# Optimization experiments

Hardware: AMD Instinct MI355X
Metric: run time of the kernel (lower is better)

The kernel has to match this reference:

```python
import jax, jax.numpy as jnp
import numpy as np

N_USERS = 100000
N_ITEMS = 200000
N_NODES = N_USERS + N_ITEMS
LATENT_DIM = 64
N_LAYERS = 3
NNZ = 6400000


def setup_inputs() -> dict:
    key = jax.random.key(0)
    k1, k2, k3, k4, k5 = jax.random.split(key, 5)
    user_emb = 0.1 * jax.random.normal(k1, (N_USERS, LATENT_DIM), dtype=jnp.float32)
    item_emb = 0.1 * jax.random.normal(k2, (N_ITEMS, LATENT_DIM), dtype=jnp.float32)
    rows = jax.random.randint(k3, (NNZ,), 0, N_NODES, dtype=jnp.int32)
    cols = jax.random.randint(k4, (NNZ,), 0, N_NODES, dtype=jnp.int32)
    # normalized-adjacency-like positive values
    vals = jax.random.uniform(k5, (NNZ,), dtype=jnp.float32) * 0.05
    return {"user_emb": user_emb, "item_emb": item_emb,
            "rows": rows, "cols": cols, "vals": vals}


def _spmm(rows, cols, vals, x):
    # y[r] += vals[e] * x[cols[e]]  for each edge e with rows[e]==r
    gathered = vals[:, None] * x[cols]          # [nnz, D]
    return jax.ops.segment_sum(gathered, rows, num_segments=N_NODES)


def reference(user_emb, item_emb, rows, cols, vals):
    # LightGCN.computer(): multi-hop propagation + layer mean pooling
    all_emb = jnp.concatenate([user_emb, item_emb], axis=0)   # [N, D]
    acc = all_emb
    for _ in range(N_LAYERS):
        all_emb = _spmm(rows, cols, vals, all_emb)
        acc = acc + all_emb
    light_out = acc / (N_LAYERS + 1)
    users = light_out[:N_USERS]
    items = light_out[N_USERS:]
    return users, items
```

## Files before the change

### kernel.cpp

```cpp
#include <hip/hip_runtime.h>
#include <hip/hip_bf16.h>

#define N_USERS 100000
#define N_ITEMS 200000
#define N_NODES 300000
#define DIM 64

#define TOT_ELEMS ((size_t)N_NODES * DIM)
#define TOT_F4    (TOT_ELEMS / 4)
#define USER_F4   (((size_t)N_USERS * DIM) / 4)

#define BROWS 512
#define NBUCKET ((N_NODES + BROWS - 1) / BROWS)
#define EPT 32
#define EDGES_PER_BLOCK (EPT * 256)

typedef float f4_native __attribute__((ext_vector_type(4)));

__device__ __forceinline__ float bf2f(unsigned short u) {
    return __uint_as_float((unsigned int)u << 16);
}
__device__ __forceinline__ unsigned short f2bf(float f) {
    __hip_bfloat16 h = __float2bfloat16(f);
    return *reinterpret_cast<unsigned short*>(&h);
}
__device__ __forceinline__ float lo_bf(unsigned int u) {
    return __uint_as_float(u << 16);
}
__device__ __forceinline__ float hi_bf(unsigned int u) {
    return __uint_as_float(u & 0xFFFF0000u);
}

__global__ void init_kernel(const float* __restrict__ user,
                            const float* __restrict__ item,
                            ushort4* __restrict__ xh) {
    size_t i = (size_t)blockIdx.x * blockDim.x + threadIdx.x;
    if (i >= TOT_F4) return;
    f4_native v = (i < USER_F4)
        ? __builtin_nontemporal_load((const f4_native*)user + i)
        : __builtin_nontemporal_load((const f4_native*)item + (i - USER_F4));
    ushort4 h;
    h.x = f2bf(v.x); h.y = f2bf(v.y); h.z = f2bf(v.z); h.w = f2bf(v.w);
    xh[i] = h;
}

__global__ void zero_buckets_kernel(int* __restrict__ bucket_count) {
    int i = blockIdx.x * blockDim.x + threadIdx.x;
    if (i < NBUCKET) bucket_count[i] = 0;
}

__global__ void bucket_hist_kernel(const int* __restrict__ rows,
                                   int* __restrict__ bucket_count, int nnz) {
    __shared__ int h[NBUCKET];
    int t = threadIdx.x;
    size_t base = (size_t)blockIdx.x * EDGES_PER_BLOCK;
    for (int i = t; i < NBUCKET; i += 256) h[i] = 0;
    __syncthreads();
    #pragma unroll 4
    for (int k = 0; k < EPT; ++k) {
        size_t e = base + (size_t)k * 256 + t;
        if (e < (size_t)nnz) atomicAdd(&h[rows[e] >> 9], 1);
    }
    __syncthreads();
    for (int i = t; i < NBUCKET; i += 256) {
        int c = h[i];
        if (c) atomicAdd(&bucket_count[i], c);
    }
}

__global__ void bucket_scan_kernel(const int* __restrict__ bucket_count,
                                   int* __restrict__ bucket_base,
                                   int* __restrict__ bucket_cursor, int nnz) {
    __shared__ int s[1024];
    int t = threadIdx.x;
    int orig = (t < NBUCKET) ? bucket_count[t] : 0;
    s[t] = orig;
    __syncthreads();
    for (int off = 1; off < 1024; off <<= 1) {
        int v = (t >= off) ? s[t - off] : 0;
        __syncthreads();
        s[t] += v;
        __syncthreads();
    }
    if (t < NBUCKET) {
        int excl = s[t] - orig;
        bucket_base[t]   = excl;
        bucket_cursor[t] = excl;
    }
    if (t == 0) bucket_base[NBUCKET] = nnz;
}

__global__ void binA_kernel(const int* __restrict__ rows,
                            const int* __restrict__ cols,
                            const float* __restrict__ vals,
                            int* __restrict__ bucket_cursor,
                            int2* __restrict__ binned,
                            int nnz) {
    __shared__ int  h[NBUCKET];
    __shared__ int  lstart[NBUCKET];
    __shared__ int  lcur[NBUCKET];
    __shared__ int  gbase[NBUCKET];
    __shared__ int  s[256];
    __shared__ int2 ledge[EDGES_PER_BLOCK];

    int t = threadIdx.x;
    size_t base = (size_t)blockIdx.x * EDGES_PER_BLOCK;
    int nvalid = (int)(((size_t)nnz - base < (size_t)EDGES_PER_BLOCK)
                       ? ((size_t)nnz - base) : (size_t)EDGES_PER_BLOCK);

    for (int i = t; i < NBUCKET; i += 256) h[i] = 0;
    __syncthreads();

    #pragma unroll 4
    for (int k = 0; k < EPT; ++k) {
        int e = k * 256 + t;
        if (e < nvalid) atomicAdd(&h[rows[base + e] >> 9], 1);
    }
    __syncthreads();

    int i0 = 3 * t, i1 = 3 * t + 1, i2 = 3 * t + 2;
    int c0 = (i0 < NBUCKET) ? h[i0] : 0;
    int c1 = (i1 < NBUCKET) ? h[i1] : 0;
    int c2 = (i2 < NBUCKET) ? h[i2] : 0;
    int g = c0 + c1 + c2;
    s[t] = g;
    __syncthreads();
    for (int off = 1; off < 256; off <<= 1) {
        int v = (t >= off) ? s[t - off] : 0;
        __syncthreads();
        s[t] += v;
        __syncthreads();
    }
    int excl = s[t] - g;
    if (i0 < NBUCKET) { lstart[i0] = excl;           lcur[i0] = excl; }
    if (i1 < NBUCKET) { lstart[i1] = excl + c0;      lcur[i1] = excl + c0; }
    if (i2 < NBUCKET) { lstart[i2] = excl + c0 + c1; lcur[i2] = excl + c0 + c1; }

    for (int i = t; i < NBUCKET; i += 256) {
        int c = h[i];
        gbase[i] = c ? atomicAdd(&bucket_cursor[i], c) : 0;
    }
    __syncthreads();

    #pragma unroll 4
    for (int k = 0; k < EPT; ++k) {
        int e = k * 256 + t;
        if (e < nvalid) {
            size_t ge = base + e;
            int r = rows[ge];
            int c = __builtin_nontemporal_load(cols + ge);
            float v = __builtin_nontemporal_load(vals + ge);
            int slot = atomicAdd(&lcur[r >> 9], 1);
            ledge[slot] = make_int2(((r & (BROWS - 1)) << 19) | c,
                                    __float_as_int(v));
        }
    }
    __syncthreads();

    for (int slot = t; slot < nvalid; slot += 256) {
        int lo = 0, hi = NBUCKET;
        while (hi - lo > 1) {
            int mid = (lo + hi) >> 1;
            if (lstart[mid] <= slot) lo = mid; else hi = mid;
        }
        binned[gbase[lo] + (slot - lstart[lo])] = ledge[slot];
    }
}

__global__ void binB_kernel(const int* __restrict__ bucket_base,
                            const int2* __restrict__ binned,
                            int2* __restrict__ sorted,
                            int* __restrict__ row_ptr,
                            int nnz) {
    __shared__ int cnt[BROWS];
    __shared__ int cur[BROWS];
    __shared__ int s[256];
    int b = blockIdx.x, t = threadIdx.x;
    int beg = bucket_base[b];
    int end = bucket_base[b + 1];
    int row0 = b * BROWS;
    for (int i = t; i < BROWS; i += 256) cnt[i] = 0;
    __syncthreads();
    for (int idx = beg + t; idx < end; idx += 256) {
        int lr = ((unsigned)binned[idx].x) >> 19;
        atomicAdd(&cnt[lr], 1);
    }
    __syncthreads();
    int c0 = cnt[2 * t], c1 = cnt[2 * t + 1];
    int local = c0 + c1;
    s[t] = local;
    __syncthreads();
    for (int off = 1; off < 256; off <<= 1) {
        int v = (t >= off) ? s[t - off] : 0;
        __syncthreads();
        s[t] += v;
        __syncthreads();
    }
    int excl = beg + s[t] - local;
    int r0 = row0 + 2 * t;
    if (r0 < N_NODES)     row_ptr[r0]     = excl;
    if (r0 + 1 < N_NODES) row_ptr[r0 + 1] = excl + c0;
    cur[2 * t]     = excl;
    cur[2 * t + 1] = excl + c0;
    __syncthreads();
    for (int idx = beg + t; idx < end; idx += 256) {
        int2 e = binned[idx];
        int lr  = ((unsigned)e.x) >> 19;
        int col = e.x & 0x7FFFF;
        int pos = atomicAdd(&cur[lr], 1);
        sorted[pos] = make_int2(col, e.y);
    }
    if (b == 0 && t == 0) row_ptr[N_NODES] = nnz;
}

__device__ __forceinline__ void row_accum2(int beg, int end, int l,
                                           const int2* __restrict__ sorted,
                                           const unsigned short* __restrict__ srch,
                                           float& r0, float& r1) {
    const int h4 = (l >> 5) << 2;
    const unsigned int q = (unsigned)(l & 31);
    const unsigned int* __restrict__ srcd = (const unsigned int*)srch;
    float acc0 = 0.f, acc1 = 0.f;

    for (int base = beg; base < end; base += 64) {
        int rem = end - base;
        int cnt = rem > 64 ? 64 : rem;
        int c_l = 0, v_l = 0;
        if (base + l < end) {
            unsigned long long e = __builtin_nontemporal_load(
                (const unsigned long long*)sorted + base + l);
            c_l = (int)(unsigned int)(e & 0xFFFFFFFFull);
            v_l = (int)(unsigned int)(e >> 32);
        }
        int npairs = (cnt + 1) >> 1;
        int p = 0;
        for (; p + 8 <= npairs; p += 8) {
            int i0 = h4 + (p << 3);
            int c0 = __builtin_amdgcn_ds_bpermute(i0 +  0, c_l);
            int c1 = __builtin_amdgcn_ds_bpermute(i0 +  8, c_l);
            int c2 = __builtin_amdgcn_ds_bpermute(i0 + 16, c_l);
            int c3 = __builtin_amdgcn_ds_bpermute(i0 + 24, c_l);
            int c4 = __builtin_amdgcn_ds_bpermute(i0 + 32, c_l);
            int c5 = __builtin_amdgcn_ds_bpermute(i0 + 40, c_l);
            int c6 = __builtin_amdgcn_ds_bpermute(i0 + 48, c_l);
            int c7 = __builtin_amdgcn_ds_bpermute(i0 + 56, c_l);
            unsigned int u0 = srcd[((unsigned int)c0 << 5) | q];
            unsigned int u1 = srcd[((unsigned int)c1 << 5) | q];
            unsigned int u2 = srcd[((unsigned int)c2 << 5) | q];
            unsigned int u3 = srcd[((unsigned int)c3 << 5) | q];
            unsigned int u4 = srcd[((unsigned int)c4 << 5) | q];
            unsigned int u5 = srcd[((unsigned int)c5 << 5) | q];
            unsigned int u6 = srcd[((unsigned int)c6 << 5) | q];
            unsigned int u7 = srcd[((unsigned int)c7 << 5) | q];
            float v0 = __int_as_float(__builtin_amdgcn_ds_bpermute(i0 +  0, v_l));
            float v1 = __int_as_float(__builtin_amdgcn_ds_bpermute(i0 +  8, v_l));
            float v2 = __int_as_float(__builtin_amdgcn_ds_bpermute(i0 + 16, v_l));
            float v3 = __int_as_float(__builtin_amdgcn_ds_bpermute(i0 + 24, v_l));
            float v4 = __int_as_float(__builtin_amdgcn_ds_bpermute(i0 + 32, v_l));
            float v5 = __int_as_float(__builtin_amdgcn_ds_bpermute(i0 + 40, v_l));
            float v6 = __int_as_float(__builtin_amdgcn_ds_bpermute(i0 + 48, v_l));
            float v7 = __int_as_float(__builtin_amdgcn_ds_bpermute(i0 + 56, v_l));
            acc0 = fmaf(v0, lo_bf(u0), acc0); acc1 = fmaf(v0, hi_bf(u0), acc1);
            acc0 = fmaf(v1, lo_bf(u1), acc0); acc1 = fmaf(v1, hi_bf(u1), acc1);
            acc0 = fmaf(v2, lo_bf(u2), acc0); acc1 = fmaf(v2, hi_bf(u2), acc1);
            acc0 = fmaf(v3, lo_bf(u3), acc0); acc1 = fmaf(v3, hi_bf(u3), acc1);
            acc0 = fmaf(v4, lo_bf(u4), acc0); acc1 = fmaf(v4, hi_bf(u4), acc1);
            acc0 = fmaf(v5, lo_bf(u5), acc0); acc1 = fmaf(v5, hi_bf(u5), acc1);
            acc0 = fmaf(v6, lo_bf(u6), acc0); acc1 = fmaf(v6, hi_bf(u6), acc1);
            acc0 = fmaf(v7, lo_bf(u7), acc0); acc1 = fmaf(v7, hi_bf(u7), acc1);
        }
        for (; p + 4 <= npairs; p += 4) {
            int i0 = h4 + (p << 3);
            int c0 = __builtin_amdgcn_ds_bpermute(i0 +  0, c_l);
            int c1 = __builtin_amdgcn_ds_bpermute(i0 +  8, c_l);
            int c2 = __builtin_amdgcn_ds_bpermute(i0 + 16, c_l);
            int c3 = __builtin_amdgcn_ds_bpermute(i0 + 24, c_l);
            unsigned int u0 = srcd[((unsigned int)c0 << 5) | q];
            unsigned int u1 = srcd[((unsigned int)c1 << 5) | q];
            unsigned int u2 = srcd[((unsigned int)c2 << 5) | q];
            unsigned int u3 = srcd[((unsigned int)c3 << 5) | q];
            float v0 = __int_as_float(__builtin_amdgcn_ds_bpermute(i0 +  0, v_l));
            float v1 = __int_as_float(__builtin_amdgcn_ds_bpermute(i0 +  8, v_l));
            float v2 = __int_as_float(__builtin_amdgcn_ds_bpermute(i0 + 16, v_l));
            float v3 = __int_as_float(__builtin_amdgcn_ds_bpermute(i0 + 24, v_l));
            acc0 = fmaf(v0, lo_bf(u0), acc0); acc1 = fmaf(v0, hi_bf(u0), acc1);
            acc0 = fmaf(v1, lo_bf(u1), acc0); acc1 = fmaf(v1, hi_bf(u1), acc1);
            acc0 = fmaf(v2, lo_bf(u2), acc0); acc1 = fmaf(v2, hi_bf(u2), acc1);
            acc0 = fmaf(v3, lo_bf(u3), acc0); acc1 = fmaf(v3, hi_bf(u3), acc1);
        }
        for (; p < npairs; ++p) {
            int i0 = h4 + (p << 3);
            int c0 = __builtin_amdgcn_ds_bpermute(i0, c_l);
            unsigned int u0 = srcd[((unsigned int)c0 << 5) | q];
            float v0 = __int_as_float(__builtin_amdgcn_ds_bpermute(i0, v_l));
            acc0 = fmaf(v0, lo_bf(u0), acc0);
            acc1 = fmaf(v0, hi_bf(u0), acc1);
        }
    }
    r0 = acc0 + __shfl_xor(acc0, 32);
    r1 = acc1 + __shfl_xor(acc1, 32);
}

__global__ void spmm_row_kernel(const int* __restrict__ row_ptr,
                                const int2* __restrict__ sorted,
                                const unsigned short* __restrict__ srch,
                                unsigned short* __restrict__ dsth) {
    int t = blockIdx.x * blockDim.x + threadIdx.x;
    int r = t >> 6;
    int l = t & 63;
    if (r >= N_NODES) return;
    float r0, r1;
    row_accum2(row_ptr[r], row_ptr[r + 1], l, sorted, srch, r0, r1);
    if (l < 32) {
        unsigned int pack = (unsigned int)f2bf(r0) | ((unsigned int)f2bf(r1) << 16);
        ((unsigned int*)dsth)[(size_t)r * 32 + l] = pack;
    }
}

__global__ void spmm_final_kernel(const int* __restrict__ row_ptr,
                                  const int2* __restrict__ sorted,
                                  const unsigned short* __restrict__ y2h,
                                  const unsigned short* __restrict__ y1h,
                                  const float* __restrict__ user,
                                  const float* __restrict__ item,
                                  float* __restrict__ out) {
    int t = blockIdx.x * blockDim.x + threadIdx.x;
    int r = t >> 6;
    int l = t & 63;
    if (r >= N_NODES) return;
    float r0, r1;
    row_accum2(row_ptr[r], row_ptr[r + 1], l, sorted, y2h, r0, r1);
    if (l < 32) {
        size_t didx = (size_t)r * 32 + l;
        unsigned int y1d = __builtin_nontemporal_load((const unsigned int*)y1h + didx);
        unsigned int y2d = __builtin_nontemporal_load((const unsigned int*)y2h + didx);
        const float* bp = (r < N_USERS) ? (user + 2 * didx)
                                        : (item + 2 * (didx - (size_t)N_USERS * 32));
        float b0 = __builtin_nontemporal_load(bp + 0);
        float b1 = __builtin_nontemporal_load(bp + 1);
        float o0 = 0.25f * (b0 + lo_bf(y1d) + lo_bf(y2d) + r0);
        float o1 = 0.25f * (b1 + hi_bf(y1d) + hi_bf(y2d) + r1);
        __builtin_nontemporal_store(o0, out + 2 * didx + 0);
        __builtin_nontemporal_store(o1, out + 2 * didx + 1);
    }
}

extern "C" void kernel_launch(void* const* d_in, const int* in_sizes, int n_in,
                              void* d_out, int out_size, void* d_ws, size_t ws_size,
                              hipStream_t stream) {
    const float* user = (const float*)d_in[0];
    const float* item = (const float*)d_in[1];
    const int*   rows = (const int*)d_in[2];
    const int*   cols = (const int*)d_in[3];
    const float* vals = (const float*)d_in[4];
    int nnz = in_sizes[2];

    float* out = (float*)d_out;

    char* p = (char*)d_ws;
    unsigned short* xh  = (unsigned short*)p; p += TOT_ELEMS * 2;
    unsigned short* y1h = (unsigned short*)p; p += TOT_ELEMS * 2;
    unsigned short* y2h = (unsigned short*)p; p += TOT_ELEMS * 2;
    int2* binned = (int2*)p; p += (size_t)nnz * sizeof(int2);
    int2* sorted = (int2*)p; p += (size_t)nnz * sizeof(int2);
    int* row_ptr       = (int*)p; p += (size_t)(N_NODES + 1) * 4;
    int* bucket_count  = (int*)p; p += (size_t)NBUCKET * 4;
    int* bucket_base   = (int*)p; p += (size_t)(NBUCKET + 1) * 4;
    int* bucket_cursor = (int*)p; p += (size_t)NBUCKET * 4;

    const int BLK = 256;
    int grid_elem = (int)((TOT_F4 + BLK - 1) / BLK);
    int grid_binA = (nnz + EDGES_PER_BLOCK - 1) / EDGES_PER_BLOCK;
    int grid_rows = (N_NODES * 64 + BLK - 1) / BLK;

    init_kernel<<<grid_elem, BLK, 0, stream>>>(user, item, (ushort4*)xh);

    zero_buckets_kernel<<<(NBUCKET + BLK - 1) / BLK, BLK, 0, stream>>>(bucket_count);
    bucket_hist_kernel<<<grid_binA, BLK, 0, stream>>>(rows, bucket_count, nnz);
    bucket_scan_kernel<<<1, 1024, 0, stream>>>(bucket_count, bucket_base, bucket_cursor, nnz);

    binA_kernel<<<grid_binA, BLK, 0, stream>>>(rows, cols, vals, bucket_cursor, binned, nnz);
    binB_kernel<<<NBUCKET, BLK, 0, stream>>>(bucket_base, binned, sorted, row_ptr, nnz);

    spmm_row_kernel<<<grid_rows, BLK, 0, stream>>>(row_ptr, sorted, xh,  y1h);
    spmm_row_kernel<<<grid_rows, BLK, 0, stream>>>(row_ptr, sorted, y1h, y2h);
    spmm_final_kernel<<<grid_rows, BLK, 0, stream>>>(row_ptr, sorted, y2h, y1h,
                                                     user, item, out);
}
```

Before: 813.5 us.

## Process eight rows per wavefront with 16-byte gathers in SpMM kernels

Changes the SpMM mapping from one row per 64-lane wavefront to eight rows per wavefront, with 8 lanes per row each gathering a 16-byte uint4 (8 bf16 values) per edge. Edge metadata is prefetched one batch ahead and broadcast within each 8-lane group via ds_bpermute. The aim is to cut wasted lanes on short rows (about 21 edges per row on average) and issue fewer, wider gather loads. In exchange, each wave loops to the longest of its eight rows, so rows of uneven length cause divergence, and registers per thread rise.

```diff
diff --git a/kernel.cpp b/kernel.cpp
--- a/kernel.cpp
+++ b/kernel.cpp
@@ -15,7 +15,8 @@
 #define EPT 32
 #define EDGES_PER_BLOCK (EPT * 256)
 
-typedef float f4_native __attribute__((ext_vector_type(4)));
+typedef float        f4_native __attribute__((ext_vector_type(4)));
+typedef unsigned int u4_native __attribute__((ext_vector_type(4)));
 
 __device__ __forceinline__ float bf2f(unsigned short u) {
     return __uint_as_float((unsigned int)u << 16);
@@ -213,92 +214,59 @@
     if (b == 0 && t == 0) row_ptr[N_NODES] = nnz;
 }
 
-__device__ __forceinline__ void row_accum2(int beg, int end, int l,
+__device__ __forceinline__ void row_accum8(int beg, int end, int l,
                                            const int2* __restrict__ sorted,
                                            const unsigned short* __restrict__ srch,
-                                           float& r0, float& r1) {
-    const int h4 = (l >> 5) << 2;
-    const unsigned int q = (unsigned)(l & 31);
-    const unsigned int* __restrict__ srcd = (const unsigned int*)srch;
-    float acc0 = 0.f, acc1 = 0.f;
-
-    for (int base = beg; base < end; base += 64) {
-        int rem = end - base;
-        int cnt = rem > 64 ? 64 : rem;
-        int c_l = 0, v_l = 0;
-        if (base + l < end) {
-            unsigned long long e = __builtin_nontemporal_load(
-                (const unsigned long long*)sorted + base + l);
-            c_l = (int)(unsigned int)(e & 0xFFFFFFFFull);
-            v_l = (int)(unsigned int)(e >> 32);
-        }
-        int npairs = (cnt + 1) >> 1;
-        int p = 0;
-        for (; p + 8 <= npairs; p += 8) {
-            int i0 = h4 + (p << 3);
-            int c0 = __builtin_amdgcn_ds_bpermute(i0 +  0, c_l);
-            int c1 = __builtin_amdgcn_ds_bpermute(i0 +  8, c_l);
-            int c2 = __builtin_amdgcn_ds_bpermute(i0 + 16, c_l);
-            int c3 = __builtin_amdgcn_ds_bpermute(i0 + 24, c_l);
-            int c4 = __builtin_amdgcn_ds_bpermute(i0 + 32, c_l);
-            int c5 = __builtin_amdgcn_ds_bpermute(i0 + 40, c_l);
-            int c6 = __builtin_amdgcn_ds_bpermute(i0 + 48, c_l);
-            int c7 = __builtin_amdgcn_ds_bpermute(i0 + 56, c_l);
-            unsigned int u0 = srcd[((unsigned int)c0 << 5) | q];
-            unsigned int u1 = srcd[((unsigned int)c1 << 5) | q];
-            unsigned int u2 = srcd[((unsigned int)c2 << 5) | q];
-            unsigned int u3 = srcd[((unsigned int)c3 << 5) | q];
-            unsigned int u4 = srcd[((unsigned int)c4 << 5) | q];
-            unsigned int u5 = srcd[((unsigned int)c5 << 5) | q];
-            unsigned int u6 = srcd[((unsigned int)c6 << 5) | q];
-            unsigned int u7 = srcd[((unsigned int)c7 << 5) | q];
-            float v0 = __int_as_float(__builtin_amdgcn_ds_bpermute(i0 +  0, v_l));
-            float v1 = __int_as_float(__builtin_amdgcn_ds_bpermute(i0 +  8, v_l));
-            float v2 = __int_as_float(__builtin_amdgcn_ds_bpermute(i0 + 16, v_l));
-            float v3 = __int_as_float(__builtin_amdgcn_ds_bpermute(i0 + 24, v_l));
-            float v4 = __int_as_float(__builtin_amdgcn_ds_bpermute(i0 + 32, v_l));
-            float v5 = __int_as_float(__builtin_amdgcn_ds_bpermute(i0 + 40, v_l));
-            float v6 = __int_as_float(__builtin_amdgcn_ds_bpermute(i0 + 48, v_l));
-            float v7 = __int_as_float(__builtin_amdgcn_ds_bpermute(i0 + 56, v_l));
-            acc0 = fmaf(v0, lo_bf(u0), acc0); acc1 = fmaf(v0, hi_bf(u0), acc1);
-            acc0 = fmaf(v1, lo_bf(u1), acc0); acc1 = fmaf(v1, hi_bf(u1), acc1);
-            acc0 = fmaf(v2, lo_bf(u2), acc0); acc1 = fmaf(v2, hi_bf(u2), acc1);
-            acc0 = fmaf(v3, lo_bf(u3), acc0); acc1 = fmaf(v3, hi_bf(u3), acc1);
-            acc0 = fmaf(v4, lo_bf(u4), acc0); acc1 = fmaf(v4, hi_bf(u4), acc1);
-            acc0 = fmaf(v5, lo_bf(u5), acc0); acc1 = fmaf(v5, hi_bf(u5), acc1);
-            acc0 = fmaf(v6, lo_bf(u6), acc0); acc1 = fmaf(v6, hi_bf(u6), acc1);
-            acc0 = fmaf(v7, lo_bf(u7), acc0); acc1 = fmaf(v7, hi_bf(u7), acc1);
-        }
-        for (; p + 4 <= npairs; p += 4) {
-            int i0 = h4 + (p << 3);
-            int c0 = __builtin_amdgcn_ds_bpermute(i0 +  0, c_l);
-            int c1 = __builtin_amdgcn_ds_bpermute(i0 +  8, c_l);
-            int c2 = __builtin_amdgcn_ds_bpermute(i0 + 16, c_l);
-            int c3 = __builtin_amdgcn_ds_bpermute(i0 + 24, c_l);
-            unsigned int u0 = srcd[((unsigned int)c0 << 5) | q];
-            unsigned int u1 = srcd[((unsigned int)c1 << 5) | q];
-            unsigned int u2 = srcd[((unsigned int)c2 << 5) | q];
-            unsigned int u3 = srcd[((unsigned int)c3 << 5) | q];
-            float v0 = __int_as_float(__builtin_amdgcn_ds_bpermute(i0 +  0, v_l));
-            float v1 = __int_as_float(__builtin_amdgcn_ds_bpermute(i0 +  8, v_l));
-            float v2 = __int_as_float(__builtin_amdgcn_ds_bpermute(i0 + 16, v_l));
-            float v3 = __int_as_float(__builtin_amdgcn_ds_bpermute(i0 + 24, v_l));
-            acc0 = fmaf(v0, lo_bf(u0), acc0); acc1 = fmaf(v0, hi_bf(u0), acc1);
-            acc0 = fmaf(v1, lo_bf(u1), acc0); acc1 = fmaf(v1, hi_bf(u1), acc1);
-            acc0 = fmaf(v2, lo_bf(u2), acc0); acc1 = fmaf(v2, hi_bf(u2), acc1);
-            acc0 = fmaf(v3, lo_bf(u3), acc0); acc1 = fmaf(v3, hi_bf(u3), acc1);
-        }
-        for (; p < npairs; ++p) {
-            int i0 = h4 + (p << 3);
-            int c0 = __builtin_amdgcn_ds_bpermute(i0, c_l);
-            unsigned int u0 = srcd[((unsigned int)c0 << 5) | q];
-            float v0 = __int_as_float(__builtin_amdgcn_ds_bpermute(i0, v_l));
-            acc0 = fmaf(v0, lo_bf(u0), acc0);
-            acc1 = fmaf(v0, hi_bf(u0), acc1);
-        }
-    }
-    r0 = acc0 + __shfl_xor(acc0, 32);
-    r1 = acc1 + __shfl_xor(acc1, 32);
+                                           float* acc) {
+    const int e7   = l & 7;
+    const int idxb = (l & ~7) << 2;
+    const uint4* __restrict__ src4 = (const uint4*)srch;
+
+    int len = end - beg;
+    int m = len;
+    m = max(m, __shfl_xor(m, 8));
+    m = max(m, __shfl_xor(m, 16));
+    m = max(m, __shfl_xor(m, 32));
+    int nb = (m + 7) >> 3;
+    if (nb <= 0) return;
+
+    int cc = 0, vc = 0;
+    {
+        int e = beg + e7;
+        if (e < end) {
+            unsigned long long ed = __builtin_nontemporal_load(
+                (const unsigned long long*)sorted + e);
+            cc = (int)(unsigned int)(ed & 0xFFFFFFFFull);
+            vc = (int)(unsigned int)(ed >> 32);
+        }
+    }
+    for (int b = 0; b < nb; ++b) {
+        int cn = 0, vn = 0;
+        if (b + 1 < nb) {
+            int e = beg + ((b + 1) << 3) + e7;
+            if (e < end) {
+                unsigned long long ed = __builtin_nontemporal_load(
+                    (const unsigned long long*)sorted + e);
+                cn = (int)(unsigned int)(ed & 0xFFFFFFFFull);
+                vn = (int)(unsigned int)(ed >> 32);
+            }
+        }
+        #pragma unroll
+        for (int j = 0; j < 8; ++j) {
+            int   c = __builtin_amdgcn_ds_bpermute(idxb + (j << 2), cc);
+            float v = __int_as_float(__builtin_amdgcn_ds_bpermute(idxb + (j << 2), vc));
+            uint4 u = src4[(size_t)(((unsigned)c << 3) | (unsigned)e7)];
+            acc[0] = fmaf(v, lo_bf(u.x), acc[0]);
+            acc[1] = fmaf(v, hi_bf(u.x), acc[1]);
+            acc[2] = fmaf(v, lo_bf(u.y), acc[2]);
+            acc[3] = fmaf(v, hi_bf(u.y), acc[3]);
+            acc[4] = fmaf(v, lo_bf(u.z), acc[4]);
+            acc[5] = fmaf(v, hi_bf(u.z), acc[5]);
+            acc[6] = fmaf(v, lo_bf(u.w), acc[6]);
+            acc[7] = fmaf(v, hi_bf(u.w), acc[7]);
+        }
+        cc = cn; vc = vn;
+    }
 }
 
 __global__ void spmm_row_kernel(const int* __restrict__ row_ptr,
@@ -306,15 +274,18 @@
                                 const unsigned short* __restrict__ srch,
                                 unsigned short* __restrict__ dsth) {
     int t = blockIdx.x * blockDim.x + threadIdx.x;
-    int r = t >> 6;
+    int w = t >> 6;
     int l = t & 63;
+    int r = w * 8 + (l >> 3);
     if (r >= N_NODES) return;
-    float r0, r1;
-    row_accum2(row_ptr[r], row_ptr[r + 1], l, sorted, srch, r0, r1);
-    if (l < 32) {
-        unsigned int pack = (unsigned int)f2bf(r0) | ((unsigned int)f2bf(r1) << 16);
-        ((unsigned int*)dsth)[(size_t)r * 32 + l] = pack;
-    }
+    float acc[8] = {0.f, 0.f, 0.f, 0.f, 0.f, 0.f, 0.f, 0.f};
+    row_accum8(row_ptr[r], row_ptr[r + 1], l, sorted, srch, acc);
+    uint4 o;
+    o.x = (unsigned)f2bf(acc[0]) | ((unsigned)f2bf(acc[1]) << 16);
+    o.y = (unsigned)f2bf(acc[2]) | ((unsigned)f2bf(acc[3]) << 16);
+    o.z = (unsigned)f2bf(acc[4]) | ((unsigned)f2bf(acc[5]) << 16);
+    o.w = (unsigned)f2bf(acc[6]) | ((unsigned)f2bf(acc[7]) << 16);
+    ((uint4*)dsth)[(size_t)r * 8 + (l & 7)] = o;
 }
 
 __global__ void spmm_final_kernel(const int* __restrict__ row_ptr,
@@ -325,24 +296,34 @@
                                   const float* __restrict__ item,
                                   float* __restrict__ out) {
     int t = blockIdx.x * blockDim.x + threadIdx.x;
-    int r = t >> 6;
+    int w = t >> 6;
     int l = t & 63;
+    int r = w * 8 + (l >> 3);
     if (r >= N_NODES) return;
-    float r0, r1;
-    row_accum2(row_ptr[r], row_ptr[r + 1], l, sorted, y2h, r0, r1);
-    if (l < 32) {
-        size_t didx = (size_t)r * 32 + l;
-        unsigned int y1d = __builtin_nontemporal_load((const unsigned int*)y1h + didx);
-        unsigned int y2d = __builtin_nontemporal_load((const unsigned int*)y2h + didx);
-        const float* bp = (r < N_USERS) ? (user + 2 * didx)
-                                        : (item + 2 * (didx - (size_t)N_USERS * 32));
-        float b0 = __builtin_nontemporal_load(bp + 0);
-        float b1 = __builtin_nontemporal_load(bp + 1);
-        float o0 = 0.25f * (b0 + lo_bf(y1d) + lo_bf(y2d) + r0);
-        float o1 = 0.25f * (b1 + hi_bf(y1d) + hi_bf(y2d) + r1);
-        __builtin_nontemporal_store(o0, out + 2 * didx + 0);
-        __builtin_nontemporal_store(o1, out + 2 * didx + 1);
-    }
+    float acc[8] = {0.f, 0.f, 0.f, 0.f, 0.f, 0.f, 0.f, 0.f};
+    row_accum8(row_ptr[r], row_ptr[r + 1], l, sorted, y2h, acc);
+
+    int e7 = l & 7;
+    size_t q4 = (size_t)r * 8 + e7;
+    u4_native y1q = __builtin_nontemporal_load((const u4_native*)y1h + q4);
+    u4_native y2q = __builtin_nontemporal_load((const u4_native*)y2h + q4);
+    size_t fidx = (size_t)r * 16 + 2 * e7;
+    const f4_native* bp = (r < N_USERS)
+        ? ((const f4_native*)user + fidx)
+        : ((const f4_native*)item + (fidx - (size_t)N_USERS * 16));
+    f4_native b0 = __builtin_nontemporal_load(bp);
+    f4_native b1 = __builtin_nontemporal_load(bp + 1);
+    f4_native o0, o1;
+    o0.x = 0.25f * (b0.x + lo_bf(y1q.x) + lo_bf(y2q.x) + acc[0]);
+    o0.y = 0.25f * (b0.y + hi_bf(y1q.x) + hi_bf(y2q.x) + acc[1]);
+    o0.z = 0.25f * (b0.z + lo_bf(y1q.y) + lo_bf(y2q.y) + acc[2]);
+    o0.w = 0.25f * (b0.w + hi_bf(y1q.y) + hi_bf(y2q.y) + acc[3]);
+    o1.x = 0.25f * (b1.x + lo_bf(y1q.z) + lo_bf(y2q.z) + acc[4]);
+    o1.y = 0.25f * (b1.y + hi_bf(y1q.z) + hi_bf(y2q.z) + acc[5]);
+    o1.z = 0.25f * (b1.z + lo_bf(y1q.w) + lo_bf(y2q.w) + acc[6]);
+    o1.w = 0.25f * (b1.w + hi_bf(y1q.w) + hi_bf(y2q.w) + acc[7]);
+    __builtin_nontemporal_store(o0, (f4_native*)out + fidx);
+    __builtin_nontemporal_store(o1, (f4_native*)out + fidx + 1);
 }
 
 extern "C" void kernel_launch(void* const* d_in, const int* in_sizes, int n_in,
@@ -371,7 +352,7 @@
     const int BLK = 256;
     int grid_elem = (int)((TOT_F4 + BLK - 1) / BLK);
     int grid_binA = (nnz + EDGES_PER_BLOCK - 1) / EDGES_PER_BLOCK;
-    int grid_rows = (N_NODES * 64 + BLK - 1) / BLK;
+    int grid_spmm = (int)(((size_t)(N_NODES / 8) * 64 + BLK - 1) / BLK);
 
     init_kernel<<<grid_elem, BLK, 0, stream>>>(user, item, (ushort4*)xh);
 
@@ -382,8 +363,8 @@
     binA_kernel<<<grid_binA, BLK, 0, stream>>>(rows, cols, vals, bucket_cursor, binned, nnz);
     binB_kernel<<<NBUCKET, BLK, 0, stream>>>(bucket_base, binned, sorted, row_ptr, nnz);
 
-    spmm_row_kernel<<<grid_rows, BLK, 0, stream>>>(row_ptr, sorted, xh,  y1h);
-    spmm_row_kernel<<<grid_rows, BLK, 0, stream>>>(row_ptr, sorted, y1h, y2h);
-    spmm_final_kernel<<<grid_rows, BLK, 0, stream>>>(row_ptr, sorted, y2h, y1h,
+    spmm_row_kernel<<<grid_spmm, BLK, 0, stream>>>(row_ptr, sorted, xh,  y1h);
+    spmm_row_kernel<<<grid_spmm, BLK, 0, stream>>>(row_ptr, sorted, y1h, y2h);
+    spmm_final_kernel<<<grid_spmm, BLK, 0, stream>>>(row_ptr, sorted, y2h, y1h,
                                                      user, item, out);
 }
```

Result: faster. 786.6 us (-3.3%).
